# Kernel tuning notes

Hardware: AMD Instinct MI355X
Metric: run time of the kernel (lower is better)

The kernel has to match this reference:

```python
import jax, jax.numpy as jnp
import numpy as np

N_NODES = 100000

def setup_inputs() -> dict:
    key = jax.random.key(0)
    k1, k2, k3 = jax.random.split(key, 3)
    x = jax.random.normal(k1, (N_NODES, 128), dtype=jnp.float32)
    edge_index = jax.random.randint(k2, (2, 1600000), 0, N_NODES, dtype=jnp.int64)
    W = jax.random.normal(k3, (128, 128), dtype=jnp.float32) * 0.05  # Linear weight [out, in]
    b = jnp.zeros((128,), dtype=jnp.float32)
    return {"x": x, "edge_index": edge_index, "W": W, "b": b}

def reference(x, edge_index, W, b):
    # GCNConv (PyG defaults): normalize=True, add_self_loops=True, bias=True.
    N = x.shape[0]
    # 1) linear transform (no bias inside)
    h = x @ W.T  # [N, H]
    # 2) add self loops
    loops = jnp.arange(N, dtype=edge_index.dtype)
    src = jnp.concatenate([edge_index[0], loops])  # source (x_j)
    dst = jnp.concatenate([edge_index[1], loops])  # target (aggregation)
    # 3) symmetric degree normalization: deg over target nodes with unit weights
    deg = jax.ops.segment_sum(jnp.ones_like(dst, dtype=h.dtype), dst, num_segments=N)
    dinv = jnp.where(deg > 0, jax.lax.rsqrt(deg), 0.0)
    norm = dinv[src] * dinv[dst]  # [E+N]
    # 4) gather-scale-scatter aggregation
    msgs = h[src] * norm[:, None]  # [E+N, H]
    out = jax.ops.segment_sum(msgs, dst, num_segments=N)
    # 5) bias
    return out + b
```

## Files before the change

kernel.cpp:

```cpp
#include <hip/hip_runtime.h>

#define H 128
#define KE 16
#define TILE (256 * KE)
#define LINB 512
#define NSUBMAX 784
#define SCAP 3072

typedef __attribute__((ext_vector_type(8))) short short8_t;
typedef __attribute__((ext_vector_type(4))) float float4_t;

__device__ __forceinline__ ushort f2bf(float f) {
  uint u = __float_as_uint(f);
  u += 0x7fff + ((u >> 16) & 1);
  return (ushort)(u >> 16);
}
__device__ __forceinline__ float bflo(uint v) { return __uint_as_float(v << 16); }
__device__ __forceinline__ float bfhi(uint v) { return __uint_as_float(v & 0xffff0000u); }

__global__ __launch_bounds__(256) void k_linbin(const float* __restrict__ x, const float* __restrict__ W,
                                                ushort* __restrict__ hs,
                                                const int* __restrict__ src, const int* __restrict__ dst,
                                                int* cur2, int* __restrict__ bsub,
                                                int N, int E, int nsubt) {
  __shared__ int cnt[NSUBMAX];
  __shared__ int lbase[NSUBMAX];
  __shared__ int gbase[NSUBMAX];
  __shared__ int ls[256];
  __shared__ int staged[TILE];
  __shared__ ushort sstage[TILE];
  const int tid = threadIdx.x;

  if (blockIdx.x < LINB) {
    const int lane = tid & 63;
    const int wid  = tid >> 6;
    const int rg   = wid >> 1;
    const int cg   = wid & 1;
    const int q    = lane >> 4;
    const int lm   = lane & 15;

    short8_t bfr[4][4];
    #pragma unroll
    for (int kk = 0; kk < 4; ++kk) {
      #pragma unroll
      for (int nf = 0; nf < 4; ++nf) {
        const float* wp = W + (cg * 64 + nf * 16 + lm) * 128 + kk * 32 + q * 8;
        float4_t w0 = *(const float4_t*)wp;
        float4_t w1 = *(const float4_t*)(wp + 4);
        union { short8_t s; ushort u[8]; } t;
        t.u[0] = f2bf(w0.x); t.u[1] = f2bf(w0.y); t.u[2] = f2bf(w0.z); t.u[3] = f2bf(w0.w);
        t.u[4] = f2bf(w1.x); t.u[5] = f2bf(w1.y); t.u[6] = f2bf(w1.z); t.u[7] = f2bf(w1.w);
        bfr[kk][nf] = t.s;
      }
    }

    const int ntiles = (N + 31) / 32;
    for (int tile = blockIdx.x; tile < ntiles; tile += LINB) {
      const int n0 = tile * 32;
      const int arow = n0 + rg * 16 + lm;
      const int arow_c = (arow < N) ? arow : (N - 1);
      const float* xp = x + (long)arow_c * H + q * 8;
      short8_t afr[4];
      #pragma unroll
      for (int kk = 0; kk < 4; ++kk) {
        float4_t x0 = *(const float4_t*)(xp + kk * 32);
        float4_t x1 = *(const float4_t*)(xp + kk * 32 + 4);
        union { short8_t s; ushort u[8]; } t;
        t.u[0] = f2bf(x0.x); t.u[1] = f2bf(x0.y); t.u[2] = f2bf(x0.z); t.u[3] = f2bf(x0.w);
        t.u[4] = f2bf(x1.x); t.u[5] = f2bf(x1.y); t.u[6] = f2bf(x1.z); t.u[7] = f2bf(x1.w);
        afr[kk] = t.s;
      }

      float4_t acc[4];
      #pragma unroll
      for (int nf = 0; nf < 4; ++nf) acc[nf] = (float4_t){0.f, 0.f, 0.f, 0.f};
      #pragma unroll
      for (int kk = 0; kk < 4; ++kk) {
        #pragma unroll
        for (int nf = 0; nf < 4; ++nf)
          acc[nf] = __builtin_amdgcn_mfma_f32_16x16x32_bf16(bfr[kk][nf], afr[kk], acc[nf], 0, 0, 0);
      }

      if (arow < N) {
        ushort* hrow = hs + (size_t)arow * H + cg * 64 + q * 4;
        #pragma unroll
        for (int nf = 0; nf < 4; ++nf) {
          uint2 o;
          o.x = (uint)f2bf(acc[nf][0]) | ((uint)f2bf(acc[nf][1]) << 16);
          o.y = (uint)f2bf(acc[nf][2]) | ((uint)f2bf(acc[nf][3]) << 16);
          *(uint2*)(hrow + nf * 16) = o;
        }
      }
    }
  } else {
    const int bb = blockIdx.x - LINB;
    for (int i = tid; i < NSUBMAX; i += 256) cnt[i] = 0;
    __syncthreads();

    const int base = bb * TILE;
    int pk[KE], off[KE];
    short sd[KE];
    #pragma unroll
    for (int k = 0; k < KE; ++k) {
      const int e = base + k * 256 + tid;
      if (e < E) {
        const int s = src[e], d = dst[e];
        const int sid = d >> 7;
        pk[k] = (s << 7) | (d & 127);
        sd[k] = (short)sid;
        off[k] = atomicAdd(&cnt[sid], 1);
      } else sd[k] = -1;
    }
    __syncthreads();

    int tsum = 0;
    if (tid < NSUBMAX / 4) {
      #pragma unroll
      for (int j = 0; j < 4; ++j) tsum += cnt[4 * tid + j];
    }
    ls[tid] = tsum;
    __syncthreads();
    for (int o = 1; o < 256; o <<= 1) {
      int v = (tid >= o) ? ls[tid - o] : 0;
      __syncthreads();
      ls[tid] += v;
      __syncthreads();
    }
    const int tot = ls[255];
    if (tid < NSUBMAX / 4) {
      int b = ls[tid] - tsum;
      #pragma unroll
      for (int j = 0; j < 4; ++j) { lbase[4 * tid + j] = b; b += cnt[4 * tid + j]; }
    }
    __syncthreads();
    for (int i = tid; i < nsubt; i += 256) {
      const int c = cnt[i];
      gbase[i] = c ? atomicAdd(&cur2[i], c) : 0;
    }
    __syncthreads();
    #pragma unroll
    for (int k = 0; k < KE; ++k) {
      if (sd[k] >= 0) {
        const int p = lbase[sd[k]] + off[k];
        staged[p] = pk[k];
        sstage[p] = (ushort)sd[k];
      }
    }
    __syncthreads();
    for (int i = tid; i < tot; i += 256) {
      const int sid = sstage[i];
      const int p = gbase[sid] + (i - lbase[sid]);
      if (p < SCAP) bsub[(size_t)sid * SCAP + p] = staged[i];
    }
  }
}

__global__ __launch_bounds__(256) void k_fill3(const int* __restrict__ bsub, const int* __restrict__ cur2,
                                               float* __restrict__ dinv, uint4* __restrict__ rowinfo,
                                               int* __restrict__ csr, int N) {
  __shared__ int cnt[128], pre[128], lcur[128];
  __shared__ int stage[SCAP], sorted[SCAP];
  const int tid = threadIdx.x;
  const int sid = blockIdx.x;
  const int gn0 = sid * 128;
  int nodes = N - gn0; if (nodes > 128) nodes = 128;
  if (nodes <= 0) return;
  if (tid < 128) cnt[tid] = 0;
  __syncthreads();

  const int slotbase = sid * SCAP;
  const int cc = min(cur2[sid], SCAP);
  const int* bp = bsub + (size_t)slotbase;
  for (int i = tid; i < cc; i += 256) {
    const int v = bp[i];
    stage[i] = v;
    atomicAdd(&cnt[v & 127], 1);
  }
  __syncthreads();

  if (tid < 128) pre[tid] = cnt[tid];
  __syncthreads();
  for (int off = 1; off < 128; off <<= 1) {
    int v = 0;
    if (tid < 128 && tid >= off) v = pre[tid - off];
    __syncthreads();
    if (tid < 128) pre[tid] += v;
    __syncthreads();
  }
  if (tid < 128) pre[tid] -= cnt[tid];
  __syncthreads();

  if (tid < nodes) {
    const int c = cnt[tid];
    const float dv = rsqrtf((float)(1 + c));
    dinv[gn0 + tid] = dv;
    rowinfo[gn0 + tid] = make_uint4((uint)(slotbase + pre[tid]), (uint)c, __float_as_uint(dv), 0u);
    lcur[tid] = pre[tid];
  }
  __syncthreads();

  for (int i = tid; i < cc; i += 256) {
    const int v = stage[i];
    const int p = atomicAdd(&lcur[v & 127], 1);
    sorted[p] = (int)((unsigned)v >> 7);
  }
  __syncthreads();
  for (int i = tid; i < cc; i += 256) csr[slotbase + i] = sorted[i];
}

#define ACCS(q, ds) { a0 = fmaf(bflo((q).x), ds, a0); a1 = fmaf(bfhi((q).x), ds, a1); \
                      a2 = fmaf(bflo((q).y), ds, a2); a3 = fmaf(bfhi((q).y), ds, a3); \
                      a4 = fmaf(bflo((q).z), ds, a4); a5 = fmaf(bfhi((q).z), ds, a5); \
                      a6 = fmaf(bflo((q).w), ds, a6); a7 = fmaf(bfhi((q).w), ds, a7); }
__global__ __launch_bounds__(256) void k_agg(const ushort* __restrict__ hs, const float* __restrict__ dinv,
                                             const uint4* __restrict__ rowinfo, const int* __restrict__ csr,
                                             const float* __restrict__ bias, float* __restrict__ out, int N) {
  const int d = blockIdx.x * 16 + (threadIdx.x >> 4);
  if (d >= N) return;
  const int j = threadIdx.x & 15;
  const uint4* hp = (const uint4*)hs;

  const uint4 info = rowinfo[d];
  int i = (int)info.x;
  int cnt = (int)info.y;
  const float dd = __uint_as_float(info.z);

  const uint4 qs = hp[(size_t)d * 16 + j];
  float a0 = bflo(qs.x) * dd, a1 = bfhi(qs.x) * dd, a2 = bflo(qs.y) * dd, a3 = bfhi(qs.y) * dd;
  float a4 = bflo(qs.z) * dd, a5 = bfhi(qs.z) * dd, a6 = bflo(qs.w) * dd, a7 = bfhi(qs.w) * dd;

  for (; cnt >= 8; cnt -= 8, i += 8) {
    const int s0 = csr[i],     s1 = csr[i + 1], s2 = csr[i + 2], s3 = csr[i + 3];
    const int s4 = csr[i + 4], s5 = csr[i + 5], s6 = csr[i + 6], s7 = csr[i + 7];
    const float d0 = dinv[s0], d1 = dinv[s1], d2 = dinv[s2], d3 = dinv[s3];
    const float d4 = dinv[s4], d5 = dinv[s5], d6 = dinv[s6], d7 = dinv[s7];
    const uint4 qA = hp[(size_t)s0 * 16 + j];
    const uint4 qB = hp[(size_t)s1 * 16 + j];
    const uint4 qC = hp[(size_t)s2 * 16 + j];
    const uint4 qD = hp[(size_t)s3 * 16 + j];
    const uint4 qE = hp[(size_t)s4 * 16 + j];
    const uint4 qF = hp[(size_t)s5 * 16 + j];
    const uint4 qG = hp[(size_t)s6 * 16 + j];
    const uint4 qH = hp[(size_t)s7 * 16 + j];
    ACCS(qA, d0) ACCS(qB, d1) ACCS(qC, d2) ACCS(qD, d3)
    ACCS(qE, d4) ACCS(qF, d5) ACCS(qG, d6) ACCS(qH, d7)
  }
  if (cnt >= 4) {
    const int s0 = csr[i], s1 = csr[i + 1], s2 = csr[i + 2], s3 = csr[i + 3];
    const float d0 = dinv[s0], d1 = dinv[s1], d2 = dinv[s2], d3 = dinv[s3];
    const uint4 qA = hp[(size_t)s0 * 16 + j];
    const uint4 qB = hp[(size_t)s1 * 16 + j];
    const uint4 qC = hp[(size_t)s2 * 16 + j];
    const uint4 qD = hp[(size_t)s3 * 16 + j];
    ACCS(qA, d0) ACCS(qB, d1) ACCS(qC, d2) ACCS(qD, d3)
    cnt -= 4; i += 4;
  }
  for (; cnt > 0; --cnt, ++i) {
    const int s = csr[i];
    const float ds = dinv[s];
    const uint4 q = hp[(size_t)s * 16 + j];
    ACCS(q, ds)
  }

  const float4_t b0 = *(const float4_t*)(bias + j * 8);
  const float4_t b1 = *(const float4_t*)(bias + j * 8 + 4);
  float4_t o0, o1;
  o0.x = a0 * dd + b0.x; o0.y = a1 * dd + b0.y; o0.z = a2 * dd + b0.z; o0.w = a3 * dd + b0.w;
  o1.x = a4 * dd + b1.x; o1.y = a5 * dd + b1.y; o1.z = a6 * dd + b1.z; o1.w = a7 * dd + b1.w;
  __builtin_nontemporal_store(o0, (float4_t*)(out + (size_t)d * H + j * 8));
  __builtin_nontemporal_store(o1, (float4_t*)(out + (size_t)d * H + j * 8 + 4));
}

extern "C" void kernel_launch(void* const* d_in, const int* in_sizes, int n_in,
                              void* d_out, int out_size, void* d_ws, size_t ws_size,
                              hipStream_t stream) {
  const float* x = (const float*)d_in[0];
  const int*   edge = (const int*)d_in[1];
  const float* W = (const float*)d_in[2];
  const float* b = (const float*)d_in[3];
  float* out = (float*)d_out;

  const int N = in_sizes[0] / H;
  const int E = in_sizes[1] / 2;
  const int* src = edge;
  const int* dst = edge + E;
  const int nsubt = (N + 127) / 128;

  char* w = (char*)d_ws;
  ushort* hs     = (ushort*)w;  w += (size_t)N * H * 2;
  float*  dinv   = (float*)w;   w += (size_t)N * 4;
  int*    cur2   = (int*)w;     w += (size_t)NSUBMAX * 4;
  uint4*  rowinfo= (uint4*)w;   w += (size_t)N * 16;
  int*    csr    = (int*)w;     w += (size_t)nsubt * SCAP * 4;
  int*    bsub   = (int*)w;     w += (size_t)nsubt * SCAP * 4;
  (void)ws_size;

  (void)hipMemsetAsync(cur2, 0, (size_t)NSUBMAX * 4, stream);

  const int nbin = (E + TILE - 1) / TILE;
  k_linbin<<<LINB + nbin, 256, 0, stream>>>(x, W, hs, src, dst, cur2, bsub, N, E, nsubt);
  k_fill3<<<nsubt, 256, 0, stream>>>(bsub, cur2, dinv, rowinfo, csr, N);
  k_agg<<<(N + 15) / 16, 256, 0, stream>>>(hs, dinv, rowinfo, csr, b, out, N);
}
```

Before: 122.3 us.

## Split linear transform across binning and fill kernels to balance overlap

```diff
diff --git a/kernel.cpp b/kernel.cpp
--- a/kernel.cpp
+++ b/kernel.cpp
@@ -18,11 +18,74 @@
 __device__ __forceinline__ float bflo(uint v) { return __uint_as_float(v << 16); }
 __device__ __forceinline__ float bfhi(uint v) { return __uint_as_float(v & 0xffff0000u); }
 
-__global__ __launch_bounds__(256) void k_linbin(const float* __restrict__ x, const float* __restrict__ W,
-                                                ushort* __restrict__ hs,
-                                                const int* __restrict__ src, const int* __restrict__ dst,
-                                                int* cur2, int* __restrict__ bsub,
-                                                int N, int E, int nsubt) {
+__device__ __forceinline__ void linear_range(const float* __restrict__ x, const float* __restrict__ W,
+                                             ushort* __restrict__ hs, int N,
+                                             int tile0, int tend, int tid) {
+  const int lane = tid & 63;
+  const int wid  = tid >> 6;
+  const int rg   = wid >> 1;
+  const int cg   = wid & 1;
+  const int q    = lane >> 4;
+  const int lm   = lane & 15;
+
+  short8_t bfr[4][4];
+  #pragma unroll
+  for (int kk = 0; kk < 4; ++kk) {
+    #pragma unroll
+    for (int nf = 0; nf < 4; ++nf) {
+      const float* wp = W + (cg * 64 + nf * 16 + lm) * 128 + kk * 32 + q * 8;
+      float4_t w0 = *(const float4_t*)wp;
+      float4_t w1 = *(const float4_t*)(wp + 4);
+      union { short8_t s; ushort u[8]; } t;
+      t.u[0] = f2bf(w0.x); t.u[1] = f2bf(w0.y); t.u[2] = f2bf(w0.z); t.u[3] = f2bf(w0.w);
+      t.u[4] = f2bf(w1.x); t.u[5] = f2bf(w1.y); t.u[6] = f2bf(w1.z); t.u[7] = f2bf(w1.w);
+      bfr[kk][nf] = t.s;
+    }
+  }
+
+  for (int tile = tile0; tile < tend; tile += LINB) {
+    const int n0 = tile * 32;
+    const int arow = n0 + rg * 16 + lm;
+    const int arow_c = (arow < N) ? arow : (N - 1);
+    const float* xp = x + (long)arow_c * H + q * 8;
+    short8_t afr[4];
+    #pragma unroll
+    for (int kk = 0; kk < 4; ++kk) {
+      float4_t x0 = *(const float4_t*)(xp + kk * 32);
+      float4_t x1 = *(const float4_t*)(xp + kk * 32 + 4);
+      union { short8_t s; ushort u[8]; } t;
+      t.u[0] = f2bf(x0.x); t.u[1] = f2bf(x0.y); t.u[2] = f2bf(x0.z); t.u[3] = f2bf(x0.w);
+      t.u[4] = f2bf(x1.x); t.u[5] = f2bf(x1.y); t.u[6] = f2bf(x1.z); t.u[7] = f2bf(x1.w);
+      afr[kk] = t.s;
+    }
+
+    float4_t acc[4];
+    #pragma unroll
+    for (int nf = 0; nf < 4; ++nf) acc[nf] = (float4_t){0.f, 0.f, 0.f, 0.f};
+    #pragma unroll
+    for (int kk = 0; kk < 4; ++kk) {
+      #pragma unroll
+      for (int nf = 0; nf < 4; ++nf)
+        acc[nf] = __builtin_amdgcn_mfma_f32_16x16x32_bf16(bfr[kk][nf], afr[kk], acc[nf], 0, 0, 0);
+    }
+
+    if (arow < N) {
+      ushort* hrow = hs + (size_t)arow * H + cg * 64 + q * 4;
+      #pragma unroll
+      for (int nf = 0; nf < 4; ++nf) {
+        uint2 o;
+        o.x = (uint)f2bf(acc[nf][0]) | ((uint)f2bf(acc[nf][1]) << 16);
+        o.y = (uint)f2bf(acc[nf][2]) | ((uint)f2bf(acc[nf][3]) << 16);
+        *(uint2*)(hrow + nf * 16) = o;
+      }
+    }
+  }
+}
+
+__global__ __launch_bounds__(256) void k_binlinA(const int* __restrict__ src, const int* __restrict__ dst,
+                                                 int* cur2, int* __restrict__ bsub, int E, int nsubt, int nbin,
+                                                 const float* __restrict__ x, const float* __restrict__ W,
+                                                 ushort* __restrict__ hs, int N, int tsplit) {
   __shared__ int cnt[NSUBMAX];
   __shared__ int lbase[NSUBMAX];
   __shared__ int gbase[NSUBMAX];
@@ -31,136 +94,85 @@
   __shared__ ushort sstage[TILE];
   const int tid = threadIdx.x;
 
-  if (blockIdx.x < LINB) {
-    const int lane = tid & 63;
-    const int wid  = tid >> 6;
-    const int rg   = wid >> 1;
-    const int cg   = wid & 1;
-    const int q    = lane >> 4;
-    const int lm   = lane & 15;
-
-    short8_t bfr[4][4];
-    #pragma unroll
-    for (int kk = 0; kk < 4; ++kk) {
-      #pragma unroll
-      for (int nf = 0; nf < 4; ++nf) {
-        const float* wp = W + (cg * 64 + nf * 16 + lm) * 128 + kk * 32 + q * 8;
-        float4_t w0 = *(const float4_t*)wp;
-        float4_t w1 = *(const float4_t*)(wp + 4);
-        union { short8_t s; ushort u[8]; } t;
-        t.u[0] = f2bf(w0.x); t.u[1] = f2bf(w0.y); t.u[2] = f2bf(w0.z); t.u[3] = f2bf(w0.w);
-        t.u[4] = f2bf(w1.x); t.u[5] = f2bf(w1.y); t.u[6] = f2bf(w1.z); t.u[7] = f2bf(w1.w);
-        bfr[kk][nf] = t.s;
-      }
-    }
-
-    const int ntiles = (N + 31) / 32;
-    for (int tile = blockIdx.x; tile < ntiles; tile += LINB) {
-      const int n0 = tile * 32;
-      const int arow = n0 + rg * 16 + lm;
-      const int arow_c = (arow < N) ? arow : (N - 1);
-      const float* xp = x + (long)arow_c * H + q * 8;
-      short8_t afr[4];
-      #pragma unroll
-      for (int kk = 0; kk < 4; ++kk) {
-        float4_t x0 = *(const float4_t*)(xp + kk * 32);
-        float4_t x1 = *(const float4_t*)(xp + kk * 32 + 4);
-        union { short8_t s; ushort u[8]; } t;
-        t.u[0] = f2bf(x0.x); t.u[1] = f2bf(x0.y); t.u[2] = f2bf(x0.z); t.u[3] = f2bf(x0.w);
-        t.u[4] = f2bf(x1.x); t.u[5] = f2bf(x1.y); t.u[6] = f2bf(x1.z); t.u[7] = f2bf(x1.w);
-        afr[kk] = t.s;
-      }
-
-      float4_t acc[4];
-      #pragma unroll
-      for (int nf = 0; nf < 4; ++nf) acc[nf] = (float4_t){0.f, 0.f, 0.f, 0.f};
-      #pragma unroll
-      for (int kk = 0; kk < 4; ++kk) {
-        #pragma unroll
-        for (int nf = 0; nf < 4; ++nf)
-          acc[nf] = __builtin_amdgcn_mfma_f32_16x16x32_bf16(bfr[kk][nf], afr[kk], acc[nf], 0, 0, 0);
-      }
-
-      if (arow < N) {
-        ushort* hrow = hs + (size_t)arow * H + cg * 64 + q * 4;
-        #pragma unroll
-        for (int nf = 0; nf < 4; ++nf) {
-          uint2 o;
-          o.x = (uint)f2bf(acc[nf][0]) | ((uint)f2bf(acc[nf][1]) << 16);
-          o.y = (uint)f2bf(acc[nf][2]) | ((uint)f2bf(acc[nf][3]) << 16);
-          *(uint2*)(hrow + nf * 16) = o;
-        }
-      }
-    }
-  } else {
-    const int bb = blockIdx.x - LINB;
-    for (int i = tid; i < NSUBMAX; i += 256) cnt[i] = 0;
+  if (blockIdx.x >= nbin) {
+    linear_range(x, W, hs, N, blockIdx.x - nbin, tsplit, tid);
+    return;
+  }
+
+  for (int i = tid; i < NSUBMAX; i += 256) cnt[i] = 0;
+  __syncthreads();
+
+  const int base = blockIdx.x * TILE;
+  int pk[KE], off[KE];
+  short sd[KE];
+  #pragma unroll
+  for (int k = 0; k < KE; ++k) {
+    const int e = base + k * 256 + tid;
+    if (e < E) {
+      const int s = src[e], d = dst[e];
+      const int sid = d >> 7;
+      pk[k] = (s << 7) | (d & 127);
+      sd[k] = (short)sid;
+      off[k] = atomicAdd(&cnt[sid], 1);
+    } else sd[k] = -1;
+  }
+  __syncthreads();
+
+  int tsum = 0;
+  if (tid < NSUBMAX / 4) {
+    #pragma unroll
+    for (int j = 0; j < 4; ++j) tsum += cnt[4 * tid + j];
+  }
+  ls[tid] = tsum;
+  __syncthreads();
+  for (int o = 1; o < 256; o <<= 1) {
+    int v = (tid >= o) ? ls[tid - o] : 0;
     __syncthreads();
-
-    const int base = bb * TILE;
-    int pk[KE], off[KE];
-    short sd[KE];
-    #pragma unroll
-    for (int k = 0; k < KE; ++k) {
-      const int e = base + k * 256 + tid;
-      if (e < E) {
-        const int s = src[e], d = dst[e];
-        const int sid = d >> 7;
-        pk[k] = (s << 7) | (d & 127);
-        sd[k] = (short)sid;
-        off[k] = atomicAdd(&cnt[sid], 1);
-      } else sd[k] = -1;
-    }
+    ls[tid] += v;
     __syncthreads();
-
-    int tsum = 0;
-    if (tid < NSUBMAX / 4) {
-      #pragma unroll
-      for (int j = 0; j < 4; ++j) tsum += cnt[4 * tid + j];
-    }
-    ls[tid] = tsum;
-    __syncthreads();
-    for (int o = 1; o < 256; o <<= 1) {
-      int v = (tid >= o) ? ls[tid - o] : 0;
-      __syncthreads();
-      ls[tid] += v;
-      __syncthreads();
-    }
-    const int tot = ls[255];
-    if (tid < NSUBMAX / 4) {
-      int b = ls[tid] - tsum;
-      #pragma unroll
-      for (int j = 0; j < 4; ++j) { lbase[4 * tid + j] = b; b += cnt[4 * tid + j]; }
-    }
-    __syncthreads();
-    for (int i = tid; i < nsubt; i += 256) {
-      const int c = cnt[i];
-      gbase[i] = c ? atomicAdd(&cur2[i], c) : 0;
-    }
-    __syncthreads();
-    #pragma unroll
-    for (int k = 0; k < KE; ++k) {
-      if (sd[k] >= 0) {
-        const int p = lbase[sd[k]] + off[k];
-        staged[p] = pk[k];
-        sstage[p] = (ushort)sd[k];
-      }
-    }
-    __syncthreads();
-    for (int i = tid; i < tot; i += 256) {
-      const int sid = sstage[i];
-      const int p = gbase[sid] + (i - lbase[sid]);
-      if (p < SCAP) bsub[(size_t)sid * SCAP + p] = staged[i];
-    }
-  }
-}
-
-__global__ __launch_bounds__(256) void k_fill3(const int* __restrict__ bsub, const int* __restrict__ cur2,
-                                               float* __restrict__ dinv, uint4* __restrict__ rowinfo,
-                                               int* __restrict__ csr, int N) {
+  }
+  const int tot = ls[255];
+  if (tid < NSUBMAX / 4) {
+    int b = ls[tid] - tsum;
+    #pragma unroll
+    for (int j = 0; j < 4; ++j) { lbase[4 * tid + j] = b; b += cnt[4 * tid + j]; }
+  }
+  __syncthreads();
+  for (int i = tid; i < nsubt; i += 256) {
+    const int c = cnt[i];
+    gbase[i] = c ? atomicAdd(&cur2[i], c) : 0;
+  }
+  __syncthreads();
+  #pragma unroll
+  for (int k = 0; k < KE; ++k) {
+    if (sd[k] >= 0) {
+      const int p = lbase[sd[k]] + off[k];
+      staged[p] = pk[k];
+      sstage[p] = (ushort)sd[k];
+    }
+  }
+  __syncthreads();
+  for (int i = tid; i < tot; i += 256) {
+    const int sid = sstage[i];
+    const int p = gbase[sid] + (i - lbase[sid]);
+    if (p < SCAP) bsub[(size_t)sid * SCAP + p] = staged[i];
+  }
+}
+
+__global__ __launch_bounds__(256) void k_fill3linB(const int* __restrict__ bsub, const int* __restrict__ cur2,
+                                                   float* __restrict__ dinv, uint4* __restrict__ rowinfo,
+                                                   int* __restrict__ csr, int N, int nsubt,
+                                                   const float* __restrict__ x, const float* __restrict__ W,
+                                                   ushort* __restrict__ hs, int tsplit, int ntiles) {
   __shared__ int cnt[128], pre[128], lcur[128];
   __shared__ int stage[SCAP], sorted[SCAP];
   const int tid = threadIdx.x;
+
+  if (blockIdx.x >= nsubt) {
+    linear_range(x, W, hs, N, tsplit + (blockIdx.x - nsubt), ntiles, tid);
+    return;
+  }
+
   const int sid = blockIdx.x;
   const int gn0 = sid * 128;
   int nodes = N - gn0; if (nodes > 128) nodes = 128;
@@ -285,6 +297,8 @@
   const int* src = edge;
   const int* dst = edge + E;
   const int nsubt = (N + 127) / 128;
+  const int ntiles = (N + 31) / 32;
+  const int tsplit = (ntiles + 1) / 2;
 
   char* w = (char*)d_ws;
   ushort* hs     = (ushort*)w;  w += (size_t)N * H * 2;
@@ -298,7 +312,8 @@
   (void)hipMemsetAsync(cur2, 0, (size_t)NSUBMAX * 4, stream);
 
   const int nbin = (E + TILE - 1) / TILE;
-  k_linbin<<<LINB + nbin, 256, 0, stream>>>(x, W, hs, src, dst, cur2, bsub, N, E, nsubt);
-  k_fill3<<<nsubt, 256, 0, stream>>>(bsub, cur2, dinv, rowinfo, csr, N);
+  k_binlinA<<<nbin + LINB, 256, 0, stream>>>(src, dst, cur2, bsub, E, nsubt, nbin, x, W, hs, N, tsplit);
+  k_fill3linB<<<nsubt + LINB, 256, 0, stream>>>(bsub, cur2, dinv, rowinfo, csr, N, nsubt,
+                                                x, W, hs, tsplit, ntiles);
   k_agg<<<(N + 15) / 16, 256, 0, stream>>>(hs, dinv, rowinfo, csr, b, out, N);
 }
```

Measured after the change: 134.0 us. 1.1x slower.
